# Performance work log

Hardware: AMD Instinct MI355X
Metric: run time of the kernel (lower is better)

The kernel has to match this reference:

```python
import jax, jax.numpy as jnp
import numpy as np

IN_DIM = 256
HID = 256  # == n_qubits, required by c = f*c + i*g
SEQ = 512
BATCH = 256


def setup_inputs() -> dict:
    key = jax.random.key(0)
    ks = jax.random.split(key, 20)
    d = IN_DIM + HID
    lim = 1.0 / np.sqrt(d)
    inp = {
        "inputs": jax.random.normal(ks[0], (SEQ, BATCH, IN_DIM), dtype=jnp.float32),
        "h0": jnp.zeros((BATCH, HID), dtype=jnp.float32),
        "c0": jnp.zeros((BATCH, HID), dtype=jnp.float32),
    }
    names = ["f", "i", "u", "o"]
    for j, n in enumerate(names):
        inp["W" + n] = jax.random.uniform(ks[1 + 4 * j], (HID, d), jnp.float32, -lim, lim)
        inp["b" + n] = jax.random.uniform(ks[2 + 4 * j], (HID,), jnp.float32, -lim, lim)
        inp["theta" + n] = jax.random.normal(ks[3 + 4 * j], (HID,), dtype=jnp.float32)
        inp["scale" + n] = jax.random.uniform(ks[4 + 4 * j], (HID,), dtype=jnp.float32)
    return inp


def _qgate(z, theta, scale):
    # simulated quantum gate: sigmoid(sin(z * theta) * scale)
    return jax.nn.sigmoid(jnp.sin(z * theta) * scale)


def reference(inputs, h0, c0,
              Wf, bf, thetaf, scalef,
              Wi, bi, thetai, scalei,
              Wu, bu, thetau, scaleu,
              Wo, bo, thetao, scaleo):
    def step(carry, x):
        h, c = carry
        comb = jnp.concatenate([x, h], axis=1)  # [B, IN+HID]
        f = jax.nn.sigmoid(_qgate(comb @ Wf.T + bf, thetaf, scalef))
        i = jax.nn.sigmoid(_qgate(comb @ Wi.T + bi, thetai, scalei))
        g = jnp.tanh(_qgate(comb @ Wu.T + bu, thetau, scaleu))
        o = jax.nn.sigmoid(_qgate(comb @ Wo.T + bo, thetao, scaleo))
        c = f * c + i * g
        h = o * jnp.tanh(c)
        return (h, c), h

    (h_n, c_n), outputs = jax.lax.scan(step, (h0, c0), inputs)
    return outputs, (h_n, c_n)
```

## Files before the change

kernel.cpp:

```cpp
#include <hip/hip_runtime.h>
#include <cstdint>
#include <cstddef>


#define SEQ 512
#define BATCH 256
#define IN_DIMX 256
#define HIDN 256
#define DTOT 512

typedef float f32x4 __attribute__((ext_vector_type(4)));
typedef short s16x8 __attribute__((ext_vector_type(8)));

__device__ __forceinline__ unsigned short f2bf(float f) {
  unsigned u = __builtin_bit_cast(unsigned, f);
  u += 0x7FFFu + ((u >> 16) & 1u);
  return (unsigned short)(u >> 16);
}

__device__ __forceinline__ float sigm(float x) {
  return __builtin_amdgcn_rcpf(1.0f + __expf(-x));
}
__device__ __forceinline__ float tanh_fast(float x) {
  return 1.0f - 2.0f * __builtin_amdgcn_rcpf(1.0f + __expf(2.0f * x));
}

__global__ void qlstm_prep(const float* __restrict__ h0,
                           unsigned short* __restrict__ hbuf,
                           int* __restrict__ flags) {
  int tid = blockIdx.x * blockDim.x + threadIdx.x;
  if (tid < (SEQ + 2) * 4) flags[tid] = 0;
  int bm = tid >> 14, kc = (tid >> 9) & 31, row = (tid >> 3) & 63, j = tid & 7;
  hbuf[tid] = f2bf(h0[(bm * 64 + row) * HIDN + kc * 8 + j]);
}

__launch_bounds__(256, 1)
__global__ void qlstm_main(
    const float* __restrict__ X, const float* __restrict__ c0,
    const float* __restrict__ Wf, const float* __restrict__ bf_,
    const float* __restrict__ thf, const float* __restrict__ scf,
    const float* __restrict__ Wi, const float* __restrict__ bi_,
    const float* __restrict__ thi, const float* __restrict__ sci,
    const float* __restrict__ Wu, const float* __restrict__ bu_,
    const float* __restrict__ thu, const float* __restrict__ scu,
    const float* __restrict__ Wo, const float* __restrict__ bo_,
    const float* __restrict__ tho, const float* __restrict__ sco,
    float* __restrict__ out,
    unsigned short* __restrict__ hbuf,
    int* __restrict__ flags) {
  __shared__ __align__(16) unsigned short hA[32 * 64 * 8];

  const int tid = threadIdx.x;
  const int wave = tid >> 6;
  const int lane = tid & 63;
  const int quad = lane >> 4;
  const int col = lane & 15;
  const int bm = blockIdx.x & 3;
  const int js = blockIdx.x >> 2;

  s16x8 wx[4][8], wh[4][8];
  {
    const float* Wg[4] = {Wf, Wi, Wu, Wo};
#pragma unroll
    for (int g = 0; g < 4; ++g) {
      const float* wr = Wg[g] + (size_t)(js * 16 + col) * DTOT + quad * 8;
#pragma unroll
      for (int s = 0; s < 16; ++s) {
        float4 p0 = *(const float4*)(wr + s * 32);
        float4 p1 = *(const float4*)(wr + s * 32 + 4);
        s16x8 fr;
        fr[0] = (short)f2bf(p0.x); fr[1] = (short)f2bf(p0.y);
        fr[2] = (short)f2bf(p0.z); fr[3] = (short)f2bf(p0.w);
        fr[4] = (short)f2bf(p1.x); fr[5] = (short)f2bf(p1.y);
        fr[6] = (short)f2bf(p1.z); fr[7] = (short)f2bf(p1.w);
        if (s < 8) wx[g][s] = fr; else wh[g][s - 8] = fr;
      }
    }
  }
  float th[4], sc[4], bi[4];
  {
    const float* Tg[4] = {thf, thi, thu, tho};
    const float* Sg[4] = {scf, sci, scu, sco};
    const float* Bg[4] = {bf_, bi_, bu_, bo_};
#pragma unroll
    for (int g = 0; g < 4; ++g) {
      th[g] = Tg[g][js * 16 + col];
      sc[g] = Sg[g][js * 16 + col];
      bi[g] = Bg[g][js * 16 + col];
    }
  }

  const int browq = bm * 64 + wave * 16 + quad * 4;
  float c[4];
#pragma unroll
  for (int r = 0; r < 4; ++r)
    c[r] = c0[(size_t)(browq + r) * HIDN + js * 16 + col];

  const float* Xrow = X + (size_t)(bm * 64 + wave * 16 + col) * IN_DIMX + quad * 8;
  const int kc_out = js * 2 + (col >> 3);
  const int jsub = col & 7;

#pragma clang loop unroll(disable)
  for (int t = 0; t < SEQ; ++t) {
    float4 xv[8][2];
    {
      const float* xb = Xrow + (size_t)t * BATCH * IN_DIMX;
#pragma unroll
      for (int s = 0; s < 8; ++s) {
        xv[s][0] = *(const float4*)(xb + s * 32);
        xv[s][1] = *(const float4*)(xb + s * 32 + 4);
      }
    }
    if (t > 0) {
      if (tid == 0) {
        while (__hip_atomic_load(&flags[t * 4 + bm], __ATOMIC_ACQUIRE,
                                 __HIP_MEMORY_SCOPE_AGENT) < 16) {
          __builtin_amdgcn_s_sleep(2);
        }
      }
      __syncthreads();
    }
    {
      const unsigned short* hsrc = hbuf + ((size_t)((t & 1) * 4 + bm)) * 16384;
#pragma unroll
      for (int i = 0; i < 8; ++i) {
        int idx = i * 256 + tid;
        *(uint4*)&hA[idx * 8] = *(const uint4*)(hsrc + idx * 8);
      }
    }
    __syncthreads();

    s16x8 xf[8];
#pragma unroll
    for (int s = 0; s < 8; ++s) {
      s16x8 fr;
      fr[0] = (short)f2bf(xv[s][0].x); fr[1] = (short)f2bf(xv[s][0].y);
      fr[2] = (short)f2bf(xv[s][0].z); fr[3] = (short)f2bf(xv[s][0].w);
      fr[4] = (short)f2bf(xv[s][1].x); fr[5] = (short)f2bf(xv[s][1].y);
      fr[6] = (short)f2bf(xv[s][1].z); fr[7] = (short)f2bf(xv[s][1].w);
      xf[s] = fr;
    }

    f32x4 acc[4];
#pragma unroll
    for (int g = 0; g < 4; ++g) acc[g] = (f32x4){bi[g], bi[g], bi[g], bi[g]};

#pragma unroll
    for (int s = 0; s < 8; ++s) {
#pragma unroll
      for (int g = 0; g < 4; ++g)
        acc[g] = __builtin_amdgcn_mfma_f32_16x16x32_bf16(xf[s], wx[g][s], acc[g], 0, 0, 0);
    }
#pragma unroll
    for (int s = 0; s < 8; ++s) {
      s16x8 af = *(const s16x8*)&hA[((s * 4 + quad) * 64 + wave * 16 + col) * 8];
#pragma unroll
      for (int g = 0; g < 4; ++g)
        acc[g] = __builtin_amdgcn_mfma_f32_16x16x32_bf16(af, wh[g][s], acc[g], 0, 0, 0);
    }

    unsigned short* hdst = hbuf + ((size_t)(((t + 1) & 1) * 4 + bm)) * 16384;
    float* orow = out + (size_t)t * BATCH * HIDN;
#pragma unroll
    for (int r = 0; r < 4; ++r) {
      float fg = sigm(sigm(__sinf(acc[0][r] * th[0]) * sc[0]));
      float ig = sigm(sigm(__sinf(acc[1][r] * th[1]) * sc[1]));
      float gg = tanh_fast(sigm(__sinf(acc[2][r] * th[2]) * sc[2]));
      float og = sigm(sigm(__sinf(acc[3][r] * th[3]) * sc[3]));
      float cn = fg * c[r] + ig * gg;
      c[r] = cn;
      float hh = og * tanh_fast(cn);
      int brow = browq + r;
      orow[(size_t)brow * HIDN + js * 16 + col] = hh;
      hdst[(kc_out * 64 + (wave * 16 + quad * 4 + r)) * 8 + jsub] = f2bf(hh);
      if (t == SEQ - 1) {
        out[(size_t)SEQ * BATCH * HIDN + (size_t)brow * HIDN + js * 16 + col] = hh;
        out[(size_t)SEQ * BATCH * HIDN + (size_t)BATCH * HIDN +
            (size_t)brow * HIDN + js * 16 + col] = cn;
      }
    }
    __syncthreads();
    if (tid == 0)
      __hip_atomic_fetch_add(&flags[(t + 1) * 4 + bm], 1, __ATOMIC_RELEASE,
                             __HIP_MEMORY_SCOPE_AGENT);
  }
}

extern "C" void kernel_launch(void* const* d_in, const int* in_sizes, int n_in,
                              void* d_out, int out_size, void* d_ws, size_t ws_size,
                              hipStream_t stream) {
  (void)in_sizes; (void)n_in; (void)out_size; (void)ws_size;
  const float* X   = (const float*)d_in[0];
  const float* h0  = (const float*)d_in[1];
  const float* c0  = (const float*)d_in[2];
  const float* Wf  = (const float*)d_in[3];
  const float* bf_ = (const float*)d_in[4];
  const float* thf = (const float*)d_in[5];
  const float* scf = (const float*)d_in[6];
  const float* Wi  = (const float*)d_in[7];
  const float* bi_ = (const float*)d_in[8];
  const float* thi = (const float*)d_in[9];
  const float* sci = (const float*)d_in[10];
  const float* Wu  = (const float*)d_in[11];
  const float* bu_ = (const float*)d_in[12];
  const float* thu = (const float*)d_in[13];
  const float* scu = (const float*)d_in[14];
  const float* Wo  = (const float*)d_in[15];
  const float* bo_ = (const float*)d_in[16];
  const float* tho = (const float*)d_in[17];
  const float* sco = (const float*)d_in[18];
  float* out = (float*)d_out;

  unsigned short* hbuf = (unsigned short*)d_ws;
  int* flags = (int*)((char*)d_ws + 262144);

  hipLaunchKernelGGL(qlstm_prep, dim3(256), dim3(256), 0, stream, h0, hbuf, flags);

  hipLaunchKernelGGL(qlstm_main, dim3(64), dim3(256), 0, stream,
                     X, c0, Wf, bf_, thf, scf, Wi, bi_, thi, sci,
                     Wu, bu_, thu, scu, Wo, bo_, tho, sco,
                     out, hbuf, flags);
}
```

Measured before the change: 3.471 ms.

## Use per-producer flags, overlap input MFMAs with the wait, and read h directly

The single shared counter per batch tile becomes 16 per-producer flags. Sixteen threads poll them with relaxed loads, and each producer publishes with a plain store after draining its outstanding memory operations. The input-projection MFMAs now run before the wait, so they can overlap the inter-block synchronisation. The hidden-state LDS staging and its extra barrier are removed: each lane loads its h fragment straight from global memory with agent-scope atomic loads, and producers write packed bf16 pairs. The relaxed ordering depends on vmcnt draining and cross-XCD coherence being sufficient, and the flag array grows sixteen-fold.

```diff
diff --git a/kernel.cpp b/kernel.cpp
--- a/kernel.cpp
+++ b/kernel.cpp
@@ -29,7 +29,7 @@
                            unsigned short* __restrict__ hbuf,
                            int* __restrict__ flags) {
   int tid = blockIdx.x * blockDim.x + threadIdx.x;
-  if (tid < (SEQ + 2) * 4) flags[tid] = 0;
+  if (tid < (SEQ + 2) * 4 * 16) flags[tid] = 0;
   int bm = tid >> 14, kc = (tid >> 9) & 31, row = (tid >> 3) & 63, j = tid & 7;
   hbuf[tid] = f2bf(h0[(bm * 64 + row) * HIDN + kc * 8 + j]);
 }
@@ -48,8 +48,6 @@
     float* __restrict__ out,
     unsigned short* __restrict__ hbuf,
     int* __restrict__ flags) {
-  __shared__ __align__(16) unsigned short hA[32 * 64 * 8];
-
   const int tid = threadIdx.x;
   const int wave = tid >> 6;
   const int lane = tid & 63;
@@ -99,6 +97,7 @@
   const float* Xrow = X + (size_t)(bm * 64 + wave * 16 + col) * IN_DIMX + quad * 8;
   const int kc_out = js * 2 + (col >> 3);
   const int jsub = col & 7;
+  const int rowA = wave * 16 + col;
 
 #pragma clang loop unroll(disable)
   for (int t = 0; t < SEQ; ++t) {
@@ -111,25 +110,6 @@
         xv[s][1] = *(const float4*)(xb + s * 32 + 4);
       }
     }
-    if (t > 0) {
-      if (tid == 0) {
-        while (__hip_atomic_load(&flags[t * 4 + bm], __ATOMIC_ACQUIRE,
-                                 __HIP_MEMORY_SCOPE_AGENT) < 16) {
-          __builtin_amdgcn_s_sleep(2);
-        }
-      }
-      __syncthreads();
-    }
-    {
-      const unsigned short* hsrc = hbuf + ((size_t)((t & 1) * 4 + bm)) * 16384;
-#pragma unroll
-      for (int i = 0; i < 8; ++i) {
-        int idx = i * 256 + tid;
-        *(uint4*)&hA[idx * 8] = *(const uint4*)(hsrc + idx * 8);
-      }
-    }
-    __syncthreads();
-
     s16x8 xf[8];
 #pragma unroll
     for (int s = 0; s < 8; ++s) {
@@ -151,15 +131,40 @@
       for (int g = 0; g < 4; ++g)
         acc[g] = __builtin_amdgcn_mfma_f32_16x16x32_bf16(xf[s], wx[g][s], acc[g], 0, 0, 0);
     }
-#pragma unroll
-    for (int s = 0; s < 8; ++s) {
-      s16x8 af = *(const s16x8*)&hA[((s * 4 + quad) * 64 + wave * 16 + col) * 8];
-#pragma unroll
-      for (int g = 0; g < 4; ++g)
-        acc[g] = __builtin_amdgcn_mfma_f32_16x16x32_bf16(af, wh[g][s], acc[g], 0, 0, 0);
-    }
-
-    unsigned short* hdst = hbuf + ((size_t)(((t + 1) & 1) * 4 + bm)) * 16384;
+
+    if (t > 0) {
+      if (tid < 16) {
+        int* fp = flags + ((size_t)t * 4 + bm) * 16 + tid;
+        while (__hip_atomic_load(fp, __ATOMIC_RELAXED,
+                                 __HIP_MEMORY_SCOPE_AGENT) == 0) {
+          __builtin_amdgcn_s_sleep(1);
+        }
+      }
+      __syncthreads();
+    }
+
+    {
+      const unsigned short* hsrc = hbuf + ((size_t)((t & 1) * 4 + bm)) * 16384;
+      unsigned long long q[16];
+#pragma unroll
+      for (int s = 0; s < 8; ++s) {
+        unsigned long long* p = (unsigned long long*)
+            (hsrc + (size_t)((s * 4 + quad) * 64 + rowA) * 8);
+        q[2 * s]     = __hip_atomic_load(p,     __ATOMIC_RELAXED, __HIP_MEMORY_SCOPE_AGENT);
+        q[2 * s + 1] = __hip_atomic_load(p + 1, __ATOMIC_RELAXED, __HIP_MEMORY_SCOPE_AGENT);
+      }
+#pragma unroll
+      for (int s = 0; s < 8; ++s) {
+        union { unsigned long long qq[2]; s16x8 v; } u;
+        u.qq[0] = q[2 * s]; u.qq[1] = q[2 * s + 1];
+#pragma unroll
+        for (int g = 0; g < 4; ++g)
+          acc[g] = __builtin_amdgcn_mfma_f32_16x16x32_bf16(u.v, wh[g][s], acc[g], 0, 0, 0);
+      }
+    }
+
+    unsigned int* hdst32 = (unsigned int*)
+        (hbuf + ((size_t)(((t + 1) & 1) * 4 + bm)) * 16384);
     float* orow = out + (size_t)t * BATCH * HIDN;
 #pragma unroll
     for (int r = 0; r < 4; ++r) {
@@ -172,17 +177,26 @@
       float hh = og * tanh_fast(cn);
       int brow = browq + r;
       orow[(size_t)brow * HIDN + js * 16 + col] = hh;
-      hdst[(kc_out * 64 + (wave * 16 + quad * 4 + r)) * 8 + jsub] = f2bf(hh);
+      float ph = __shfl_xor(hh, 1);
+      if ((col & 1) == 0) {
+        unsigned int w = (unsigned)f2bf(hh) | ((unsigned)f2bf(ph) << 16);
+        __hip_atomic_store(
+            &hdst32[(size_t)(kc_out * 64 + wave * 16 + quad * 4 + r) * 4 + (jsub >> 1)],
+            w, __ATOMIC_RELAXED, __HIP_MEMORY_SCOPE_AGENT);
+      }
       if (t == SEQ - 1) {
         out[(size_t)SEQ * BATCH * HIDN + (size_t)brow * HIDN + js * 16 + col] = hh;
         out[(size_t)SEQ * BATCH * HIDN + (size_t)BATCH * HIDN +
             (size_t)brow * HIDN + js * 16 + col] = cn;
       }
     }
+
     __syncthreads();
-    if (tid == 0)
-      __hip_atomic_fetch_add(&flags[(t + 1) * 4 + bm], 1, __ATOMIC_RELEASE,
-                             __HIP_MEMORY_SCOPE_AGENT);
+    if (tid == 0) {
+      asm volatile("s_waitcnt vmcnt(0)" ::: "memory");
+      __hip_atomic_store(flags + ((size_t)(t + 1) * 4 + bm) * 16 + js, 1,
+                         __ATOMIC_RELAXED, __HIP_MEMORY_SCOPE_AGENT);
+    }
   }
 }
 
```

After: 3.322 ms. 4.3% less time.

## Replace flag barrier with per-word tagged h exchange polled directly

Applied to the files above, without the earlier changes.

Each exchanged hidden-state word now carries its timestep tag in the upper 32 bits of a 64-bit atomic. Consumers poll their own fragments until every tag matches, so the flag counter, the single-thread spin, the block-wide syncthreads and the LDS staging copy are all gone. The h loads are issued early so they overlap the X-part MFMAs. The cost is double the traffic for the h exchange and repeated polling of 32 words per lane; correctness relies on 64-bit atomic stores and the double buffer not being overwritten before slower blocks read it.

```diff
diff --git a/kernel.cpp b/kernel.cpp
--- a/kernel.cpp
+++ b/kernel.cpp
@@ -26,12 +26,16 @@
 }
 
 __global__ void qlstm_prep(const float* __restrict__ h0,
-                           unsigned short* __restrict__ hbuf,
-                           int* __restrict__ flags) {
+                           unsigned long long* __restrict__ thbuf) {
   int tid = blockIdx.x * blockDim.x + threadIdx.x;
-  if (tid < (SEQ + 2) * 4) flags[tid] = 0;
-  int bm = tid >> 14, kc = (tid >> 9) & 31, row = (tid >> 3) & 63, j = tid & 7;
-  hbuf[tid] = f2bf(h0[(bm * 64 + row) * HIDN + kc * 8 + j]);
+  if (tid >= 32768) return;
+  int bm = tid >> 13, rem = tid & 8191;
+  int kc = rem >> 8, row = (rem >> 2) & 63, q = rem & 3;
+  float a = h0[(size_t)(bm * 64 + row) * HIDN + kc * 8 + q * 2];
+  float b = h0[(size_t)(bm * 64 + row) * HIDN + kc * 8 + q * 2 + 1];
+  unsigned pay = (unsigned)f2bf(a) | ((unsigned)f2bf(b) << 16);
+  thbuf[tid] = (unsigned long long)pay;
+  thbuf[32768 + tid] = 0xFFFFFFFF00000000ull;
 }
 
 __launch_bounds__(256, 1)
@@ -46,10 +50,7 @@
     const float* __restrict__ Wo, const float* __restrict__ bo_,
     const float* __restrict__ tho, const float* __restrict__ sco,
     float* __restrict__ out,
-    unsigned short* __restrict__ hbuf,
-    int* __restrict__ flags) {
-  __shared__ __align__(16) unsigned short hA[32 * 64 * 8];
-
+    unsigned long long* __restrict__ thbuf) {
   const int tid = threadIdx.x;
   const int wave = tid >> 6;
   const int lane = tid & 63;
@@ -99,9 +100,24 @@
   const float* Xrow = X + (size_t)(bm * 64 + wave * 16 + col) * IN_DIMX + quad * 8;
   const int kc_out = js * 2 + (col >> 3);
   const int jsub = col & 7;
+  const int rowA = wave * 16 + col;
 
 #pragma clang loop unroll(disable)
   for (int t = 0; t < SEQ; ++t) {
+    const unsigned long long* hsrc =
+        thbuf + ((size_t)((t & 1) * 4 + bm)) * 8192;
+
+    unsigned long long q64[32];
+#pragma unroll
+    for (int s = 0; s < 8; ++s) {
+      const unsigned long long* p =
+          hsrc + ((size_t)((s * 4 + quad) * 64 + rowA)) * 4;
+#pragma unroll
+      for (int j = 0; j < 4; ++j)
+        q64[s * 4 + j] = __hip_atomic_load(p + j, __ATOMIC_RELAXED,
+                                           __HIP_MEMORY_SCOPE_AGENT);
+    }
+
     float4 xv[8][2];
     {
       const float* xb = Xrow + (size_t)t * BATCH * IN_DIMX;
@@ -111,25 +127,6 @@
         xv[s][1] = *(const float4*)(xb + s * 32 + 4);
       }
     }
-    if (t > 0) {
-      if (tid == 0) {
-        while (__hip_atomic_load(&flags[t * 4 + bm], __ATOMIC_ACQUIRE,
-                                 __HIP_MEMORY_SCOPE_AGENT) < 16) {
-          __builtin_amdgcn_s_sleep(2);
-        }
-      }
-      __syncthreads();
-    }
-    {
-      const unsigned short* hsrc = hbuf + ((size_t)((t & 1) * 4 + bm)) * 16384;
-#pragma unroll
-      for (int i = 0; i < 8; ++i) {
-        int idx = i * 256 + tid;
-        *(uint4*)&hA[idx * 8] = *(const uint4*)(hsrc + idx * 8);
-      }
-    }
-    __syncthreads();
-
     s16x8 xf[8];
 #pragma unroll
     for (int s = 0; s < 8; ++s) {
@@ -151,16 +148,38 @@
       for (int g = 0; g < 4; ++g)
         acc[g] = __builtin_amdgcn_mfma_f32_16x16x32_bf16(xf[s], wx[g][s], acc[g], 0, 0, 0);
     }
-#pragma unroll
-    for (int s = 0; s < 8; ++s) {
-      s16x8 af = *(const s16x8*)&hA[((s * 4 + quad) * 64 + wave * 16 + col) * 8];
+
+    {
+      const unsigned long long want = (unsigned long long)(unsigned)t;
+      for (;;) {
+        unsigned bad = 0;
+#pragma unroll
+        for (int i = 0; i < 32; ++i)
+          bad |= (unsigned)((q64[i] >> 32) != want);
+        if (!bad) break;
+#pragma unroll
+        for (int s = 0; s < 8; ++s) {
+          const unsigned long long* p =
+              hsrc + ((size_t)((s * 4 + quad) * 64 + rowA)) * 4;
+#pragma unroll
+          for (int j = 0; j < 4; ++j)
+            q64[s * 4 + j] = __hip_atomic_load(p + j, __ATOMIC_RELAXED,
+                                               __HIP_MEMORY_SCOPE_AGENT);
+        }
+      }
+    }
+
+#pragma unroll
+    for (int s = 0; s < 8; ++s) {
+      union { unsigned w[4]; s16x8 v; } fu;
+#pragma unroll
+      for (int j = 0; j < 4; ++j) fu.w[j] = (unsigned)q64[s * 4 + j];
 #pragma unroll
       for (int g = 0; g < 4; ++g)
-        acc[g] = __builtin_amdgcn_mfma_f32_16x16x32_bf16(af, wh[g][s], acc[g], 0, 0, 0);
-    }
-
-    unsigned short* hdst = hbuf + ((size_t)(((t + 1) & 1) * 4 + bm)) * 16384;
-    float* orow = out + (size_t)t * BATCH * HIDN;
+        acc[g] = __builtin_amdgcn_mfma_f32_16x16x32_bf16(fu.v, wh[g][s], acc[g], 0, 0, 0);
+    }
+
+    float hh[4];
 #pragma unroll
     for (int r = 0; r < 4; ++r) {
       float fg = sigm(sigm(__sinf(acc[0][r] * th[0]) * sc[0]));
@@ -169,20 +188,41 @@
       float og = sigm(sigm(__sinf(acc[3][r] * th[3]) * sc[3]));
       float cn = fg * c[r] + ig * gg;
       c[r] = cn;
-      float hh = og * tanh_fast(cn);
-      int brow = browq + r;
-      orow[(size_t)brow * HIDN + js * 16 + col] = hh;
-      hdst[(kc_out * 64 + (wave * 16 + quad * 4 + r)) * 8 + jsub] = f2bf(hh);
-      if (t == SEQ - 1) {
-        out[(size_t)SEQ * BATCH * HIDN + (size_t)brow * HIDN + js * 16 + col] = hh;
-        out[(size_t)SEQ * BATCH * HIDN + (size_t)BATCH * HIDN +
-            (size_t)brow * HIDN + js * 16 + col] = cn;
-      }
-    }
-    __syncthreads();
-    if (tid == 0)
-      __hip_atomic_fetch_add(&flags[(t + 1) * 4 + bm], 1, __ATOMIC_RELEASE,
-                             __HIP_MEMORY_SCOPE_AGENT);
+      hh[r] = og * tanh_fast(cn);
+    }
+
+    {
+      unsigned long long* hdst =
+          thbuf + ((size_t)(((t + 1) & 1) * 4 + bm)) * 8192;
+      const unsigned long long tagv =
+          ((unsigned long long)(unsigned)(t + 1)) << 32;
+#pragma unroll
+      for (int r = 0; r < 4; ++r) {
+        float ph = __shfl_xor(hh[r], 1);
+        if ((col & 1) == 0) {
+          unsigned pay = (unsigned)f2bf(hh[r]) | ((unsigned)f2bf(ph) << 16);
+          __hip_atomic_store(
+              hdst + ((size_t)(kc_out * 64 + wave * 16 + quad * 4 + r)) * 4 +
+                  (jsub >> 1),
+              (unsigned long long)pay | tagv,
+              __ATOMIC_RELAXED, __HIP_MEMORY_SCOPE_AGENT);
+        }
+      }
+    }
+
+    {
+      float* orow = out + (size_t)t * BATCH * HIDN;
+#pragma unroll
+      for (int r = 0; r < 4; ++r) {
+        int brow = browq + r;
+        orow[(size_t)brow * HIDN + js * 16 + col] = hh[r];
+        if (t == SEQ - 1) {
+          out[(size_t)SEQ * BATCH * HIDN + (size_t)brow * HIDN + js * 16 + col] = hh[r];
+          out[(size_t)SEQ * BATCH * HIDN + (size_t)BATCH * HIDN +
+              (size_t)brow * HIDN + js * 16 + col] = c[r];
+        }
+      }
+    }
   }
 }
 
@@ -211,13 +251,12 @@
   const float* sco = (const float*)d_in[18];
   float* out = (float*)d_out;
 
-  unsigned short* hbuf = (unsigned short*)d_ws;
-  int* flags = (int*)((char*)d_ws + 262144);
-
-  hipLaunchKernelGGL(qlstm_prep, dim3(256), dim3(256), 0, stream, h0, hbuf, flags);
+  unsigned long long* thbuf = (unsigned long long*)d_ws;
+
+  hipLaunchKernelGGL(qlstm_prep, dim3(256), dim3(256), 0, stream, h0, thbuf);
 
   hipLaunchKernelGGL(qlstm_main, dim3(64), dim3(256), 0, stream,
                      X, c0, Wf, bf_, thf, scf, Wi, bi_, thi, sci,
                      Wu, bu_, thu, scu, Wo, bo_, tho, sco,
-                     out, hbuf, flags);
-}
+                     out, thbuf);
+}
```

Result: slower. 4.114 ms (+18.5%).
